# Optimization experiments

Hardware: AMD Instinct MI355X
Metric: run time of the kernel (lower is better)

The kernel has to match this reference:

```python
import jax, jax.numpy as jnp
import numpy as np

B, T, D, V = 32, 2048, 256, 2048  # batch, time, embed_dim, num_codebooks


def setup_inputs() -> dict:
    key = jax.random.key(0)
    k1, k2 = jax.random.split(key)
    z = jax.random.normal(k1, (B, T, D), dtype=jnp.float32)
    codebook_weight = jax.random.normal(k2, (V, D), dtype=jnp.float32)
    return {"z": z, "codebook_weight": codebook_weight}


def reference(z, codebook_weight):
    # e = codebook.embedding.weight.clone().detach()
    e = jax.lax.stop_gradient(codebook_weight)            # (V, D)
    zf = z.reshape(-1, e.shape[1])                        # (N, D), N = B*T
    # squared euclidean distances via GEMM expansion
    d = (jnp.sum(zf * zf, axis=1, keepdims=True)
         + jnp.sum(e * e, axis=1)
         - 2.0 * zf @ e.T)                                # (N, V)
    idx = jnp.argmin(d, axis=1)                           # (N,)
    # one-hot matmul with e is mathematically a row gather of e
    z_q = jnp.take(e, idx, axis=0).reshape(z.shape)       # (B, T, D)
    commitment_loss = jnp.mean((z - jax.lax.stop_gradient(z_q)) ** 2)
    z_q_st = z + jax.lax.stop_gradient(z_q - z)           # straight-through
    encoding_indices = idx.reshape(z.shape[0], z.shape[1])  # (B, T)
    hist = jnp.bincount(idx, length=V).astype(jnp.float32)
    codebook_prob = hist / (hist.sum() + 1e-8)
    return commitment_loss, z_q_st, encoding_indices, codebook_prob
```

## Files before the change

### kernel.cpp

```cpp
#include <hip/hip_runtime.h>

#define NROWS 65536
#define DIM   256
#define VCB   2048

typedef _Float16 f16;
typedef _Float16 f16x8 __attribute__((ext_vector_type(8)));
typedef float    f32x4 __attribute__((ext_vector_type(4)));


__device__ __forceinline__ void async16(void* lds, const void* g) {
  __builtin_amdgcn_global_load_lds(
      (const __attribute__((address_space(1))) void*)g,
      (__attribute__((address_space(3))) void*)lds, 16, 0, 0);
}

__global__ __launch_bounds__(256) void convert_kernel(
    const float4* __restrict__ src, short4* __restrict__ dhi,
    short4* __restrict__ dlo, int n4) {
  int stride = gridDim.x * 256;
  for (int i = blockIdx.x * 256 + threadIdx.x; i < n4; i += stride) {
    float4 v = src[i];
    union { f16 h[4]; short4 s; } H, L;
    H.h[0] = (f16)v.x; H.h[1] = (f16)v.y; H.h[2] = (f16)v.z; H.h[3] = (f16)v.w;
    L.h[0] = (f16)(v.x - (float)H.h[0]);
    L.h[1] = (f16)(v.y - (float)H.h[1]);
    L.h[2] = (f16)(v.z - (float)H.h[2]);
    L.h[3] = (f16)(v.w - (float)H.h[3]);
    dhi[i] = H.s; dlo[i] = L.s;
  }
}

__global__ __launch_bounds__(256) void prep_kernel(
    const float* __restrict__ e, float* __restrict__ enorm,
    unsigned int* __restrict__ hist, double* __restrict__ loss_part) {
  int tid = threadIdx.x;
  int gt = blockIdx.x * 256 + tid;
  if (gt < VCB) hist[gt] = 0u;
  if (gt < 256) loss_part[gt] = 0.0;
  int wid  = gt >> 6;
  int lane = tid & 63;
  if (wid < VCB) {
    const float4* row = (const float4*)(e + (size_t)wid * DIM);
    float4 v = row[lane];
    float s = v.x*v.x + v.y*v.y + v.z*v.z + v.w*v.w;
    #pragma unroll
    for (int off = 32; off; off >>= 1) s += __shfl_xor(s, off);
    if (lane == 0) enorm[wid] = s;
  }
}

__global__ __launch_bounds__(512) void argmin_kernel(
    const float* __restrict__ z,
    const f16* __restrict__ eh, const f16* __restrict__ el,
    const float* __restrict__ enorm,
    int* __restrict__ idx_out, unsigned int* __restrict__ hist,
    double* __restrict__ loss_part) {
  __shared__ f16 ldsA[8][8192];
  __shared__ f16 ldsB[2][8192];

  const int tid  = threadIdx.x;
  const int wid  = tid >> 6;
  const int lane = tid & 63;
  const int wr   = wid >> 2;
  const int wc   = wid & 3;
  const int lrow = lane & 15;
  const int lq   = lane >> 4;
  const int rbase = blockIdx.x * 128;

  const int srow = tid >> 2;
  const int scol = tid & 3;
  const int skoff = ((scol ^ ((srow >> 1) & 3)) << 3);

  auto stageB = [&](int b, int vcol, int kt) {
    size_t off = (size_t)(vcol + srow) * DIM + (kt << 5) + skoff;
    async16(&ldsB[b][0]    + tid * 8, eh + off);
    async16(&ldsB[b][4096] + tid * 8, el + off);
  };

  {
    const int row = tid >> 2;
    const int q   = tid & 3;
    const float* zrow = z + (size_t)(rbase + row) * DIM + q * 64;
    const int sw = (row >> 1) & 3;
    float zs = 0.f;
    #pragma unroll
    for (int f = 0; f < 16; ++f) {
      float4 v = *(const float4*)(zrow + f * 4);
      int col4   = q * 64 + f * 4;
      int kt     = col4 >> 5;
      int ko     = col4 & 31;
      int chunk  = ko >> 3;
      int within = (ko & 7) * 2;
      int addr = kt * 16384 + row * 64 + ((chunk ^ sw) << 4) + within;
      union { f16 h[4]; short4 s4; } H, L;
      H.h[0] = (f16)v.x; H.h[1] = (f16)v.y; H.h[2] = (f16)v.z; H.h[3] = (f16)v.w;
      L.h[0] = (f16)(v.x - (float)H.h[0]);
      L.h[1] = (f16)(v.y - (float)H.h[1]);
      L.h[2] = (f16)(v.z - (float)H.h[2]);
      L.h[3] = (f16)(v.w - (float)H.h[3]);
      *(short4*)((char*)ldsA + addr)        = H.s4;
      *(short4*)((char*)ldsA + addr + 8192) = L.s4;
      zs += v.x*v.x + v.y*v.y + v.z*v.z + v.w*v.w;
    }
    #pragma unroll
    for (int off = 32; off; off >>= 1) zs += __shfl_xor(zs, off);
    if (lane == 0) atomicAdd(&loss_part[blockIdx.x & 255], (double)zs);
  }
  stageB(0, 0, 0);
  asm volatile("s_waitcnt vmcnt(0)" ::: "memory");
  __syncthreads();

  float minv[4][4];
  int   mini[4][4];
  #pragma unroll
  for (int m = 0; m < 4; ++m)
    #pragma unroll
    for (int r = 0; r < 4; ++r) { minv[m][r] = 3.4e38f; mini[m][r] = 0; }

  const int cchunk = lq ^ ((lrow >> 1) & 3);

  int pb = 0;
  for (int ss = 0; ss < 4; ++ss) {
    const int vt = ss << 9;
    f32x4 acc[4][4][2];
    #pragma unroll
    for (int h = 0; h < 4; ++h)
      #pragma unroll
      for (int m = 0; m < 4; ++m)
        #pragma unroll
        for (int n = 0; n < 2; ++n) {
          f32x4 zz = {0.f, 0.f, 0.f, 0.f};
          acc[h][m][n] = zz;
        }

    f16x8 ah[4], al[4];
    for (int kt = 0; kt < 8; ++kt) {
      #pragma unroll
      for (int h = 0; h < 4; ++h) {
        bool last = (ss == 3) && (kt == 7) && (h == 3);
        if (!last) {
          int nh = h + 1, nkt = kt, nss = ss;
          if (nh == 4) { nh = 0; ++nkt; if (nkt == 8) { nkt = 0; ++nss; } }
          stageB(pb ^ 1, (nss << 9) + (nh << 7), nkt);
          asm volatile("s_waitcnt vmcnt(2)" ::: "memory");
        } else {
          asm volatile("s_waitcnt vmcnt(0)" ::: "memory");
        }
        asm volatile("s_barrier" ::: "memory");
        __builtin_amdgcn_sched_barrier(0);

        if (h == 0) {
          const char* abase = (const char*)&ldsA[kt][0];
          #pragma unroll
          for (int m = 0; m < 4; ++m) {
            int row = wr * 64 + m * 16 + lrow;
            int off = row * 64 + cchunk * 16;
            ah[m] = *(const f16x8*)(abase + off);
            al[m] = *(const f16x8*)(abase + 8192 + off);
          }
        }
        const char* bbase = (const char*)&ldsB[0][0] + pb * 16384;
        __builtin_amdgcn_s_setprio(1);
        #pragma unroll
        for (int n = 0; n < 2; ++n) {
          int col = wc * 32 + n * 16 + lrow;
          int off = col * 64 + cchunk * 16;
          f16x8 bh = *(const f16x8*)(bbase + off);
          f16x8 bl = *(const f16x8*)(bbase + 8192 + off);
          #pragma unroll
          for (int m = 0; m < 4; ++m) {
            acc[h][m][n] = __builtin_amdgcn_mfma_f32_16x16x32_f16(ah[m], bh, acc[h][m][n], 0, 0, 0);
            acc[h][m][n] = __builtin_amdgcn_mfma_f32_16x16x32_f16(ah[m], bl, acc[h][m][n], 0, 0, 0);
            acc[h][m][n] = __builtin_amdgcn_mfma_f32_16x16x32_f16(al[m], bh, acc[h][m][n], 0, 0, 0);
          }
        }
        __builtin_amdgcn_s_setprio(0);
        __builtin_amdgcn_sched_barrier(0);
        asm volatile("s_barrier" ::: "memory");
        pb ^= 1;
      }
    }

    #pragma unroll
    for (int h = 0; h < 4; ++h)
      #pragma unroll
      for (int n = 0; n < 2; ++n) {
        int j = vt + (h << 7) + wc * 32 + n * 16 + lrow;
        float en = enorm[j];
        #pragma unroll
        for (int m = 0; m < 4; ++m)
          #pragma unroll
          for (int r = 0; r < 4; ++r) {
            float s = fmaf(-2.f, acc[h][m][n][r], en);
            if (s < minv[m][r]) { minv[m][r] = s; mini[m][r] = j; }
          }
      }
  }

  #pragma unroll
  for (int off = 1; off < 16; off <<= 1) {
    #pragma unroll
    for (int m = 0; m < 4; ++m)
      #pragma unroll
      for (int r = 0; r < 4; ++r) {
        float ov = __shfl_xor(minv[m][r], off);
        int   oi = __shfl_xor(mini[m][r], off);
        if (ov < minv[m][r] || (ov == minv[m][r] && oi < mini[m][r])) {
          minv[m][r] = ov; mini[m][r] = oi;
        }
      }
  }

  __syncthreads();
  float* sxv = (float*)&ldsB[0][0];
  int*   sxi = (int*)(sxv + 3 * 2 * 64);
  if (wc != 0 && lrow == 0) {
    #pragma unroll
    for (int m = 0; m < 4; ++m)
      #pragma unroll
      for (int r = 0; r < 4; ++r) {
        int li = m * 16 + lq * 4 + r;
        int ix = ((wc - 1) * 2 + wr) * 64 + li;
        sxv[ix] = minv[m][r];
        sxi[ix] = mini[m][r];
      }
  }
  __syncthreads();
  if (wc == 0 && lrow == 0) {
    float lsum = 0.f;
    #pragma unroll
    for (int m = 0; m < 4; ++m)
      #pragma unroll
      for (int r = 0; r < 4; ++r) {
        int li = m * 16 + lq * 4 + r;
        float v  = minv[m][r];
        int   bi = mini[m][r];
        #pragma unroll
        for (int g = 0; g < 3; ++g) {
          int ix = (g * 2 + wr) * 64 + li;
          float ov = sxv[ix];
          int   oi = sxi[ix];
          if (ov < v || (ov == v && oi < bi)) { v = ov; bi = oi; }
        }
        idx_out[rbase + wr * 64 + li] = bi;
        atomicAdd(&hist[bi], 1u);
        lsum += v;
      }
    lsum += __shfl_xor(lsum, 16);
    lsum += __shfl_xor(lsum, 32);
    if (lane == 0) atomicAdd(&loss_part[blockIdx.x & 255], (double)lsum);
  }
}

__global__ __launch_bounds__(256) void gather_kernel(
    const float* __restrict__ e, const int* __restrict__ idx,
    float* __restrict__ zq_out, float* __restrict__ idxf_out) {
  int tid  = threadIdx.x;
  int w    = tid >> 6;
  int lane = tid & 63;
  int n    = blockIdx.x * 4 + w;

  int ci = idx[n];
  const float4* er = (const float4*)(e + (size_t)ci * DIM);
  ((float4*)(zq_out + (size_t)n * DIM))[lane] = er[lane];
  if (lane == 0) idxf_out[n] = (float)ci;
}

__global__ __launch_bounds__(256) void finalize_kernel(
    const unsigned int* __restrict__ hist, const double* __restrict__ loss_part,
    float* __restrict__ out) {
  __shared__ double lsh[4];
  __shared__ float  hsh[4];
  __shared__ float  denom_sh;
  int tid = threadIdx.x, lane = tid & 63, w = tid >> 6;

  float hs = 0.f;
  for (int j = tid; j < VCB; j += 256) hs += (float)hist[j];
  double ls = loss_part[tid];
  #pragma unroll
  for (int off = 32; off; off >>= 1) {
    hs += __shfl_xor(hs, off);
    ls += __shfl_xor(ls, off);
  }
  if (lane == 0) { lsh[w] = ls; hsh[w] = hs; }
  __syncthreads();
  if (tid == 0) {
    double lt = lsh[0] + lsh[1] + lsh[2] + lsh[3];
    float  ht = hsh[0] + hsh[1] + hsh[2] + hsh[3];
    out[0] = (float)(lt / (double)((size_t)NROWS * DIM));
    denom_sh = ht + 1e-8f;
  }
  __syncthreads();
  float denom = denom_sh;
  float* prob = out + 1 + (size_t)NROWS * DIM + NROWS;
  for (int j = tid; j < VCB; j += 256) prob[j] = (float)hist[j] / denom;
}

extern "C" void kernel_launch(void* const* d_in, const int* in_sizes, int n_in,
                              void* d_out, int out_size, void* d_ws, size_t ws_size,
                              hipStream_t stream) {
  (void)in_sizes; (void)n_in; (void)out_size; (void)ws_size;
  const float* z = (const float*)d_in[0];
  const float* e = (const float*)d_in[1];
  float* out = (float*)d_out;
  char*  ws  = (char*)d_ws;

  int*          idx       = (int*)ws;
  unsigned int* hist      = (unsigned int*)(ws + 262144);
  double*       loss_part = (double*)(ws + 270336);
  float*        enorm     = (float*)(ws + 272384);
  f16*          e_hi      = (f16*)(ws + 524288);
  f16*          e_lo      = (f16*)(ws + 1572864);

  float* out_zq  = out + 1;
  float* out_idx = out + 1 + (size_t)NROWS * DIM;

  convert_kernel<<<128, 256, 0, stream>>>(
      (const float4*)e, (short4*)e_hi, (short4*)e_lo, VCB * DIM / 4);
  prep_kernel<<<512, 256, 0, stream>>>(e, enorm, hist, loss_part);
  argmin_kernel<<<NROWS / 128, 512, 0, stream>>>(
      z, e_hi, e_lo, enorm, idx, hist, loss_part);
  gather_kernel<<<NROWS / 4, 256, 0, stream>>>(e, idx, out_zq, out_idx);
  finalize_kernel<<<1, 256, 0, stream>>>(hist, loss_part, out);
}
```

Baseline: 250.8 us.

## Give each wave a private codebook slice and drop block-wide barriers

Restructures the argmin kernel into 64-row blocks of 4 waves. Each wave owns 512 codebook columns and double-buffers its own B tiles in private LDS, so the per-step s_barrier pair is no longer needed. This removes barrier stalls and cross-wave synchronisation in the main MFMA loop. In exchange, the number of blocks doubles, so codebook reads from L2 double and B tiles are no longer shared between waves.

New measurement: 277.6 us. 10.7% more time.

```diff
diff --git a/kernel.cpp b/kernel.cpp
--- a/kernel.cpp
+++ b/kernel.cpp
@@ -50,33 +50,21 @@
   }
 }
 
-__global__ __launch_bounds__(512) void argmin_kernel(
+__global__ __launch_bounds__(256) void argmin_kernel(
     const float* __restrict__ z,
     const f16* __restrict__ eh, const f16* __restrict__ el,
     const float* __restrict__ enorm,
     int* __restrict__ idx_out, unsigned int* __restrict__ hist,
     double* __restrict__ loss_part) {
-  __shared__ f16 ldsA[8][8192];
-  __shared__ f16 ldsB[2][8192];
+  __shared__ f16 ldsA[8][4096];
+  __shared__ f16 ldsB[4][2][4096];
 
   const int tid  = threadIdx.x;
   const int wid  = tid >> 6;
   const int lane = tid & 63;
-  const int wr   = wid >> 2;
-  const int wc   = wid & 3;
   const int lrow = lane & 15;
   const int lq   = lane >> 4;
-  const int rbase = blockIdx.x * 128;
-
-  const int srow = tid >> 2;
-  const int scol = tid & 3;
-  const int skoff = ((scol ^ ((srow >> 1) & 3)) << 3);
-
-  auto stageB = [&](int b, int vcol, int kt) {
-    size_t off = (size_t)(vcol + srow) * DIM + (kt << 5) + skoff;
-    async16(&ldsB[b][0]    + tid * 8, eh + off);
-    async16(&ldsB[b][4096] + tid * 8, el + off);
-  };
+  const int rbase = blockIdx.x * 64;
 
   {
     const int row = tid >> 2;
@@ -92,7 +80,7 @@
       int ko     = col4 & 31;
       int chunk  = ko >> 3;
       int within = (ko & 7) * 2;
-      int addr = kt * 16384 + row * 64 + ((chunk ^ sw) << 4) + within;
+      int addr = kt * 8192 + row * 64 + ((chunk ^ sw) << 4) + within;
       union { f16 h[4]; short4 s4; } H, L;
       H.h[0] = (f16)v.x; H.h[1] = (f16)v.y; H.h[2] = (f16)v.z; H.h[3] = (f16)v.w;
       L.h[0] = (f16)(v.x - (float)H.h[0]);
@@ -100,16 +88,27 @@
       L.h[2] = (f16)(v.z - (float)H.h[2]);
       L.h[3] = (f16)(v.w - (float)H.h[3]);
       *(short4*)((char*)ldsA + addr)        = H.s4;
-      *(short4*)((char*)ldsA + addr + 8192) = L.s4;
+      *(short4*)((char*)ldsA + addr + 4096) = L.s4;
       zs += v.x*v.x + v.y*v.y + v.z*v.z + v.w*v.w;
     }
     #pragma unroll
     for (int off = 32; off; off >>= 1) zs += __shfl_xor(zs, off);
     if (lane == 0) atomicAdd(&loss_part[blockIdx.x & 255], (double)zs);
   }
-  stageB(0, 0, 0);
-  asm volatile("s_waitcnt vmcnt(0)" ::: "memory");
-  __syncthreads();
+  __syncthreads();
+
+  auto stageB = [&](int b, int cc, int kt) {
+    f16* base = &ldsB[wid][b][0];
+    const int vcol = wid * 512 + cc * 64;
+    #pragma unroll
+    for (int i = 0; i < 4; ++i) {
+      int col = i * 16 + (lane >> 2);
+      int swc = (col >> 1) & 3;
+      size_t goff = (size_t)(vcol + col) * DIM + (kt << 5) + (((lane & 3) ^ swc) << 3);
+      async16(base +        i * 512 + lane * 8, eh + goff);
+      async16(base + 2048 + i * 512 + lane * 8, el + goff);
+    }
+  };
 
   float minv[4][4];
   int   mini[4][4];
@@ -120,83 +119,72 @@
 
   const int cchunk = lq ^ ((lrow >> 1) & 3);
 
-  int pb = 0;
-  for (int ss = 0; ss < 4; ++ss) {
-    const int vt = ss << 9;
-    f32x4 acc[4][4][2];
-    #pragma unroll
-    for (int h = 0; h < 4; ++h)
+  int mybuf = 0;
+  stageB(0, 0, 0);
+
+  for (int cc = 0; cc < 8; ++cc) {
+    f32x4 acc[4][4];
+    #pragma unroll
+    for (int m = 0; m < 4; ++m)
+      #pragma unroll
+      for (int n = 0; n < 4; ++n) {
+        f32x4 zz = {0.f, 0.f, 0.f, 0.f};
+        acc[m][n] = zz;
+      }
+
+    for (int kt = 0; kt < 8; ++kt) {
+      {
+        int nkt = kt + 1, ncc = cc;
+        if (nkt == 8) { nkt = 0; ++ncc; if (ncc == 8) ncc = 0; }
+        stageB(mybuf ^ 1, ncc, nkt);
+      }
+      asm volatile("s_waitcnt vmcnt(8)" ::: "memory");
+      __builtin_amdgcn_sched_barrier(0);
+
+      const char* abase = (const char*)ldsA + kt * 8192;
+      f16x8 ah[4], al[4];
+      #pragma unroll
+      for (int m = 0; m < 4; ++m) {
+        int row = m * 16 + lrow;
+        int off = row * 64 + cchunk * 16;
+        ah[m] = *(const f16x8*)(abase + off);
+        al[m] = *(const f16x8*)(abase + 4096 + off);
+      }
+      const char* bbase = (const char*)&ldsB[wid][mybuf][0];
+      __builtin_amdgcn_s_setprio(1);
+      #pragma unroll
+      for (int n = 0; n < 4; ++n) {
+        int col = n * 16 + lrow;
+        int off = col * 64 + cchunk * 16;
+        f16x8 bh = *(const f16x8*)(bbase + off);
+        f16x8 bl = *(const f16x8*)(bbase + 4096 + off);
+        #pragma unroll
+        for (int m = 0; m < 4; ++m) {
+          acc[m][n] = __builtin_amdgcn_mfma_f32_16x16x32_f16(ah[m], bh, acc[m][n], 0, 0, 0);
+          acc[m][n] = __builtin_amdgcn_mfma_f32_16x16x32_f16(ah[m], bl, acc[m][n], 0, 0, 0);
+          acc[m][n] = __builtin_amdgcn_mfma_f32_16x16x32_f16(al[m], bh, acc[m][n], 0, 0, 0);
+        }
+      }
+      __builtin_amdgcn_s_setprio(0);
+      mybuf ^= 1;
+    }
+
+    const int cbase = wid * 512 + cc * 64;
+    #pragma unroll
+    for (int n = 0; n < 4; ++n) {
+      int j = cbase + n * 16 + lrow;
+      float en = enorm[j];
       #pragma unroll
       for (int m = 0; m < 4; ++m)
         #pragma unroll
-        for (int n = 0; n < 2; ++n) {
-          f32x4 zz = {0.f, 0.f, 0.f, 0.f};
-          acc[h][m][n] = zz;
+        for (int r = 0; r < 4; ++r) {
+          float s = fmaf(-2.f, acc[m][n][r], en);
+          if (s < minv[m][r]) { minv[m][r] = s; mini[m][r] = j; }
         }
-
-    f16x8 ah[4], al[4];
-    for (int kt = 0; kt < 8; ++kt) {
-      #pragma unroll
-      for (int h = 0; h < 4; ++h) {
-        bool last = (ss == 3) && (kt == 7) && (h == 3);
-        if (!last) {
-          int nh = h + 1, nkt = kt, nss = ss;
-          if (nh == 4) { nh = 0; ++nkt; if (nkt == 8) { nkt = 0; ++nss; } }
-          stageB(pb ^ 1, (nss << 9) + (nh << 7), nkt);
-          asm volatile("s_waitcnt vmcnt(2)" ::: "memory");
-        } else {
-          asm volatile("s_waitcnt vmcnt(0)" ::: "memory");
-        }
-        asm volatile("s_barrier" ::: "memory");
-        __builtin_amdgcn_sched_barrier(0);
-
-        if (h == 0) {
-          const char* abase = (const char*)&ldsA[kt][0];
-          #pragma unroll
-          for (int m = 0; m < 4; ++m) {
-            int row = wr * 64 + m * 16 + lrow;
-            int off = row * 64 + cchunk * 16;
-            ah[m] = *(const f16x8*)(abase + off);
-            al[m] = *(const f16x8*)(abase + 8192 + off);
-          }
-        }
-        const char* bbase = (const char*)&ldsB[0][0] + pb * 16384;
-        __builtin_amdgcn_s_setprio(1);
-        #pragma unroll
-        for (int n = 0; n < 2; ++n) {
-          int col = wc * 32 + n * 16 + lrow;
-          int off = col * 64 + cchunk * 16;
-          f16x8 bh = *(const f16x8*)(bbase + off);
-          f16x8 bl = *(const f16x8*)(bbase + 8192 + off);
-          #pragma unroll
-          for (int m = 0; m < 4; ++m) {
-            acc[h][m][n] = __builtin_amdgcn_mfma_f32_16x16x32_f16(ah[m], bh, acc[h][m][n], 0, 0, 0);
-            acc[h][m][n] = __builtin_amdgcn_mfma_f32_16x16x32_f16(ah[m], bl, acc[h][m][n], 0, 0, 0);
-            acc[h][m][n] = __builtin_amdgcn_mfma_f32_16x16x32_f16(al[m], bh, acc[h][m][n], 0, 0, 0);
-          }
-        }
-        __builtin_amdgcn_s_setprio(0);
-        __builtin_amdgcn_sched_barrier(0);
-        asm volatile("s_barrier" ::: "memory");
-        pb ^= 1;
-      }
     }
-
-    #pragma unroll
-    for (int h = 0; h < 4; ++h)
-      #pragma unroll
-      for (int n = 0; n < 2; ++n) {
-        int j = vt + (h << 7) + wc * 32 + n * 16 + lrow;
-        float en = enorm[j];
-        #pragma unroll
-        for (int m = 0; m < 4; ++m)
-          #pragma unroll
-          for (int r = 0; r < 4; ++r) {
-            float s = fmaf(-2.f, acc[h][m][n][r], en);
-            if (s < minv[m][r]) { minv[m][r] = s; mini[m][r] = j; }
-          }
-      }
-  }
+  }
+
+  asm volatile("s_waitcnt vmcnt(0)" ::: "memory");
 
   #pragma unroll
   for (int off = 1; off < 16; off <<= 1) {
@@ -213,21 +201,20 @@
   }
 
   __syncthreads();
-  float* sxv = (float*)&ldsB[0][0];
-  int*   sxi = (int*)(sxv + 3 * 2 * 64);
-  if (wc != 0 && lrow == 0) {
+  float* sxv = (float*)&ldsB[0][0][0];
+  int*   sxi = (int*)(sxv + 3 * 64);
+  if (wid != 0 && lrow == 0) {
     #pragma unroll
     for (int m = 0; m < 4; ++m)
       #pragma unroll
       for (int r = 0; r < 4; ++r) {
         int li = m * 16 + lq * 4 + r;
-        int ix = ((wc - 1) * 2 + wr) * 64 + li;
-        sxv[ix] = minv[m][r];
-        sxi[ix] = mini[m][r];
-      }
-  }
-  __syncthreads();
-  if (wc == 0 && lrow == 0) {
+        sxv[(wid - 1) * 64 + li] = minv[m][r];
+        sxi[(wid - 1) * 64 + li] = mini[m][r];
+      }
+  }
+  __syncthreads();
+  if (wid == 0 && lrow == 0) {
     float lsum = 0.f;
     #pragma unroll
     for (int m = 0; m < 4; ++m)
@@ -238,12 +225,11 @@
         int   bi = mini[m][r];
         #pragma unroll
         for (int g = 0; g < 3; ++g) {
-          int ix = (g * 2 + wr) * 64 + li;
-          float ov = sxv[ix];
-          int   oi = sxi[ix];
+          float ov = sxv[g * 64 + li];
+          int   oi = sxi[g * 64 + li];
           if (ov < v || (ov == v && oi < bi)) { v = ov; bi = oi; }
         }
-        idx_out[rbase + wr * 64 + li] = bi;
+        idx_out[rbase + li] = bi;
         atomicAdd(&hist[bi], 1u);
         lsum += v;
       }
@@ -319,7 +305,7 @@
   convert_kernel<<<128, 256, 0, stream>>>(
       (const float4*)e, (short4*)e_hi, (short4*)e_lo, VCB * DIM / 4);
   prep_kernel<<<512, 256, 0, stream>>>(e, enorm, hist, loss_part);
-  argmin_kernel<<<NROWS / 128, 512, 0, stream>>>(
+  argmin_kernel<<<NROWS / 64, 256, 0, stream>>>(
       z, e_hi, e_lo, enorm, idx, hist, loss_part);
   gather_kernel<<<NROWS / 4, 256, 0, stream>>>(e, idx, out_zq, out_idx);
   finalize_kernel<<<1, 256, 0, stream>>>(hist, loss_part, out);
```
